# Kernel tuning notes

Measured on AMD Instinct MI355X. Metric: run time of the kernel, lower is better.

The kernel has to match this reference:

```python
import jax, jax.numpy as jnp
import numpy as np

N = 16_777_216  # number of draft tokens / cache slots
ACCEPT_PROB = 0.7


def setup_inputs() -> dict:
    key = jax.random.key(0)
    k1, k2, k3 = jax.random.split(key, 3)
    idx = jax.random.randint(k1, (N,), 0, N, dtype=jnp.int64)
    keep = jax.random.uniform(k2, (N,)) < ACCEPT_PROB
    # rejected slots are marked -1, as in the original kernel
    accept_index = jnp.where(keep, idx, jnp.int64(-1))
    out_cache_loc = jax.random.normal(k3, (N,), dtype=jnp.float32)
    return {"accept_index": accept_index, "out_cache_loc": out_cache_loc}


def reference(accept_index, out_cache_loc):
    """Stream compaction: gather out_cache_loc[accept_index[i]] for every i with
    accept_index[i] >= 0, packed densely at the front of the output.

    The original returns an array of length num_accepted (data-dependent). For a
    static, jit-compatible shape we return a length-N array whose first
    num_accepted entries equal the original output and the rest are zero.
    """
    n = accept_index.shape[0]
    mask = accept_index >= 0                      # [N] bool
    # exclusive prefix sum of mask = destination slot for each accepted element
    dst = jnp.cumsum(mask.astype(jnp.int64)) - mask.astype(jnp.int64)  # [N]
    # gather (use 0 as a safe dummy index for rejected lanes)
    vals = out_cache_loc[jnp.where(mask, accept_index, 0)]             # [N]
    # scatter accepted values to their compacted slots; rejected lanes are
    # routed to index n, which mode='drop' discards
    scatter_idx = jnp.where(mask, dst, n)
    out = jnp.zeros((n,), dtype=out_cache_loc.dtype)
    out = out.at[scatter_idx].set(vals, mode="drop")
    return out
```

## Files before the change

### kernel.cpp

```cpp
#include <hip/hip_runtime.h>


#define N_TOTAL  16777216
#define BLOCK    256
#define EPT2     32
#define TILE2    (BLOCK * EPT2)
#define NB2      (N_TOTAL / TILE2)
#define SLICE_LG 20
#define SLICES   16

#define EPT      16
#define TILE     (BLOCK * EPT)
#define NBLOCKS  (N_TOTAL / TILE)
#define SLICE_LG5 22
#define SLICES5  (N_TOTAL >> SLICE_LG5)

typedef float vfloat4 __attribute__((ext_vector_type(4)));

__global__ __launch_bounds__(BLOCK) void k_count(const int* __restrict__ idx,
                                                 int* __restrict__ cnt) {
    __shared__ int h[SLICES];
    const int b = blockIdx.x, t = threadIdx.x;
    if (t < SLICES) h[t] = 0;
    __syncthreads();
    const int4* p = (const int4*)(idx + (size_t)b * TILE2 + (size_t)t * EPT2);
    int v[EPT2];
#pragma unroll
    for (int j = 0; j < EPT2 / 4; ++j) {
        int4 q = p[j];
        v[4*j+0]=q.x; v[4*j+1]=q.y; v[4*j+2]=q.z; v[4*j+3]=q.w;
    }
#pragma unroll
    for (int j = 0; j < EPT2; ++j) {
        unsigned s = (unsigned)v[j] >> SLICE_LG;
        if (s < SLICES) atomicAdd(&h[s], 1);
    }
    __syncthreads();
    if (t < SLICES) cnt[b * SLICES + t] = h[t];
}

__global__ __launch_bounds__(BLOCK) void k_scan2(const int* __restrict__ cnt,
                                                 int* __restrict__ off,
                                                 int* __restrict__ sliceBase,
                                                 int* __restrict__ blockOff) {
    const int t = threadIdx.x, lane = t & 63, wave = t >> 6;
    const int R = NB2 / BLOCK;
    int sum[SLICES];
#pragma unroll
    for (int s = 0; s < SLICES; ++s) sum[s] = 0;
    for (int r = 0; r < R; ++r) {
        const int4* row = (const int4*)(cnt + (size_t)(t * R + r) * SLICES);
        int4 c0 = row[0], c1 = row[1], c2 = row[2], c3 = row[3];
        sum[0]+=c0.x; sum[1]+=c0.y; sum[2]+=c0.z; sum[3]+=c0.w;
        sum[4]+=c1.x; sum[5]+=c1.y; sum[6]+=c1.z; sum[7]+=c1.w;
        sum[8]+=c2.x; sum[9]+=c2.y; sum[10]+=c2.z; sum[11]+=c2.w;
        sum[12]+=c3.x; sum[13]+=c3.y; sum[14]+=c3.z; sum[15]+=c3.w;
    }
    int inc[SLICES];
#pragma unroll
    for (int s = 0; s < SLICES; ++s) inc[s] = sum[s];
#pragma unroll
    for (int d = 1; d < 64; d <<= 1) {
#pragma unroll
        for (int s = 0; s < SLICES; ++s) {
            int u = __shfl_up(inc[s], d);
            if (lane >= d) inc[s] += u;
        }
    }
    int tTot = 0;
#pragma unroll
    for (int s = 0; s < SLICES; ++s) tTot += sum[s];
    int tInc = tTot;
#pragma unroll
    for (int d = 1; d < 64; d <<= 1) {
        int u = __shfl_up(tInc, d);
        if (lane >= d) tInc += u;
    }
    __shared__ int wtot[4][SLICES], wstot[4];
    __shared__ int wbase[4][SLICES], wsbase[4];
    if (lane == 63) {
#pragma unroll
        for (int s = 0; s < SLICES; ++s) wtot[wave][s] = inc[s];
        wstot[wave] = tInc;
    }
    __syncthreads();
    if (t == 0) {
        int run[SLICES];
#pragma unroll
        for (int s = 0; s < SLICES; ++s) run[s] = 0;
        for (int w = 0; w < 4; ++w)
#pragma unroll
            for (int s = 0; s < SLICES; ++s) { wbase[w][s] = run[s]; run[s] += wtot[w][s]; }
        int sr = 0;
#pragma unroll
        for (int s = 0; s < SLICES; ++s) { sliceBase[s] = sr; sr += run[s]; }
        sliceBase[SLICES] = sr;
        blockOff[NB2] = sr;
        int rs = 0;
        for (int w = 0; w < 4; ++w) { wsbase[w] = rs; rs += wstot[w]; }
    }
    __syncthreads();
    int ex[SLICES];
#pragma unroll
    for (int s = 0; s < SLICES; ++s) ex[s] = inc[s] - sum[s] + wbase[wave][s];
    int exA = tInc - tTot + wsbase[wave];
    for (int r = 0; r < R; ++r) {
        const int b = t * R + r;
        blockOff[b] = exA;
        const int4* row = (const int4*)(cnt + (size_t)b * SLICES);
        int4 c0 = row[0], c1 = row[1], c2 = row[2], c3 = row[3];
        int rv[SLICES] = {c0.x,c0.y,c0.z,c0.w, c1.x,c1.y,c1.z,c1.w,
                          c2.x,c2.y,c2.z,c2.w, c3.x,c3.y,c3.z,c3.w};
#pragma unroll
        for (int s = 0; s < SLICES; ++s) {
            off[(size_t)b * SLICES + s] = ex[s];
            ex[s] += rv[s];
            exA   += rv[s];
        }
    }
}

__global__ __launch_bounds__(BLOCK) void k_bin(const int* __restrict__ idx,
                                               const int* __restrict__ off,
                                               const int* __restrict__ sliceBase,
                                               int* __restrict__ bins) {
    const int b = blockIdx.x, t = threadIdx.x, lane = t & 63, wave = t >> 6;
    const int4* p = (const int4*)(idx + (size_t)b * TILE2 + (size_t)t * EPT2);
    int v[EPT2];
#pragma unroll
    for (int j = 0; j < EPT2 / 4; ++j) {
        int4 q = p[j];
        v[4*j+0]=q.x; v[4*j+1]=q.y; v[4*j+2]=q.z; v[4*j+3]=q.w;
    }
    int tc[SLICES];
#pragma unroll
    for (int s = 0; s < SLICES; ++s) tc[s] = 0;
#pragma unroll
    for (int j = 0; j < EPT2; ++j) {
        unsigned s = (unsigned)v[j] >> SLICE_LG;
#pragma unroll
        for (int s2 = 0; s2 < SLICES; ++s2) tc[s2] += (s == (unsigned)s2);
    }
    int inc[SLICES];
#pragma unroll
    for (int s = 0; s < SLICES; ++s) inc[s] = tc[s];
#pragma unroll
    for (int d = 1; d < 64; d <<= 1) {
#pragma unroll
        for (int s = 0; s < SLICES; ++s) {
            int u = __shfl_up(inc[s], d);
            if (lane >= d) inc[s] += u;
        }
    }
    __shared__ int wtot[4][SLICES], wbase[4][SLICES];
    __shared__ int gbase[SLICES], segStart[SLICES + 1];
    if (lane == 63)
#pragma unroll
        for (int s = 0; s < SLICES; ++s) wtot[wave][s] = inc[s];
    __syncthreads();
    if (t == 0) {
        int run[SLICES];
#pragma unroll
        for (int s = 0; s < SLICES; ++s) run[s] = 0;
        for (int w = 0; w < 4; ++w)
#pragma unroll
            for (int s = 0; s < SLICES; ++s) { wbase[w][s] = run[s]; run[s] += wtot[w][s]; }
        int sr = 0;
#pragma unroll
        for (int s = 0; s < SLICES; ++s) { segStart[s] = sr; sr += run[s]; }
        segStart[SLICES] = sr;
#pragma unroll
        for (int s = 0; s < SLICES; ++s)
            gbase[s] = sliceBase[s] + off[(size_t)b * SLICES + s] - segStart[s];
    }
    __syncthreads();
    __shared__ int exb[BLOCK][SLICES + 1];
    __shared__ int binsBuf[TILE2];
#pragma unroll
    for (int s = 0; s < SLICES; ++s)
        exb[t][s] = segStart[s] + (inc[s] - tc[s]) + wbase[wave][s];
#pragma unroll
    for (int j = 0; j < EPT2; ++j) {
        unsigned s = (unsigned)v[j] >> SLICE_LG;
        if (s < SLICES) {
            int pLoc = exb[t][s]++;
            binsBuf[pLoc] = v[j];
        }
    }
    __syncthreads();
    const int tot = segStart[SLICES];
    for (int k = t; k < tot; k += BLOCK) {
        int x = binsBuf[k];
        int s = 0;
#pragma unroll
        for (int q = 1; q < SLICES; ++q) s += (k >= segStart[q]);
        __builtin_nontemporal_store(x, bins + gbase[s] + k);
    }
}

__global__ __launch_bounds__(BLOCK) void k_gather(const int* __restrict__ bins,
                                                  const float* __restrict__ src,
                                                  const int* __restrict__ sliceBase,
                                                  float* __restrict__ val) {
    __shared__ int pad[18432];
    const int t = threadIdx.x;
    pad[t] = t;
    const int n = blockIdx.x;
    const int x = n & 7;
    const int g = n >> 9;
    const int q = (n >> 3) & 63;
    const int s = 2 * x + (g >> 1);
    const int c = (g & 1) * 64 + q;
    const int s0 = sliceBase[s], s1 = sliceBase[s + 1];
    if (s1 == -1) val[0] = (float)pad[t];
    const int len = s1 - s0;
    const int L = (len + 127) >> 7;
    const int start = s0 + c * L;
    const int end = (start + L < s1) ? (start + L) : s1;
    for (int k0 = start + t; k0 < end; k0 += BLOCK * 8) {
        int kk[8], bm[8];
        float fm[8];
#pragma unroll
        for (int m = 0; m < 8; ++m) kk[m] = k0 + m * BLOCK;
#pragma unroll
        for (int m = 0; m < 8; ++m) {
            int kc = kk[m] < end ? kk[m] : end - 1;
            bm[m] = __builtin_nontemporal_load(bins + kc);
        }
#pragma unroll
        for (int m = 0; m < 8; ++m) fm[m] = src[bm[m]];
#pragma unroll
        for (int m = 0; m < 8; ++m)
            if (kk[m] < end) __builtin_nontemporal_store(fm[m], val + kk[m]);
    }
}

__global__ __launch_bounds__(BLOCK) void k_emit(const int* __restrict__ idx,
                                                const int* __restrict__ off,
                                                const int* __restrict__ sliceBase,
                                                const int* __restrict__ blockOff,
                                                const float* __restrict__ val,
                                                float* __restrict__ out) {
    const int b = blockIdx.x, t = threadIdx.x, lane = t & 63, wave = t >> 6;
    const int4* p = (const int4*)(idx + (size_t)b * TILE2 + (size_t)t * EPT2);
    int v[EPT2];
#pragma unroll
    for (int j = 0; j < EPT2 / 4; ++j) {
        int4 q = p[j];
        v[4*j+0]=q.x; v[4*j+1]=q.y; v[4*j+2]=q.z; v[4*j+3]=q.w;
    }
    int tc[SLICES];
#pragma unroll
    for (int s = 0; s < SLICES; ++s) tc[s] = 0;
#pragma unroll
    for (int j = 0; j < EPT2; ++j) {
        unsigned s = (unsigned)v[j] >> SLICE_LG;
#pragma unroll
        for (int s2 = 0; s2 < SLICES; ++s2) tc[s2] += (s == (unsigned)s2);
    }
    int inc[SLICES];
#pragma unroll
    for (int s = 0; s < SLICES; ++s) inc[s] = tc[s];
#pragma unroll
    for (int d = 1; d < 64; d <<= 1) {
#pragma unroll
        for (int s = 0; s < SLICES; ++s) {
            int u = __shfl_up(inc[s], d);
            if (lane >= d) inc[s] += u;
        }
    }
    int cnt = 0;
#pragma unroll
    for (int s = 0; s < SLICES; ++s) cnt += tc[s];
    int xinc = cnt;
#pragma unroll
    for (int d = 1; d < 64; d <<= 1) {
        int u = __shfl_up(xinc, d);
        if (lane >= d) xinc += u;
    }
    __shared__ int wtot[4][SLICES], wbase[4][SLICES];
    __shared__ int wsum[4], woff[4], sTot;
    if (lane == 63) {
#pragma unroll
        for (int s = 0; s < SLICES; ++s) wtot[wave][s] = inc[s];
        wsum[wave] = xinc;
    }
    __syncthreads();
    if (t == 0) {
        int run[SLICES];
#pragma unroll
        for (int s = 0; s < SLICES; ++s) run[s] = 0;
        for (int w = 0; w < 4; ++w)
#pragma unroll
            for (int s = 0; s < SLICES; ++s) { wbase[w][s] = run[s]; run[s] += wtot[w][s]; }
        int rs = 0;
        for (int w = 0; w < 4; ++w) { woff[w] = rs; rs += wsum[w]; }
        sTot = rs;
    }
    __syncthreads();
    __shared__ int exb[BLOCK][SLICES + 1];
#pragma unroll
    for (int s = 0; s < SLICES; ++s)
        exb[t][s] = sliceBase[s] + off[(size_t)b * SLICES + s]
                  + (inc[s] - tc[s]) + wbase[wave][s];
    int slotA[EPT2];
#pragma unroll
    for (int j = 0; j < EPT2; ++j) {
        unsigned s = (unsigned)v[j] >> SLICE_LG;
        slotA[j] = (s < SLICES) ? exb[t][s]++ : 0;
    }
    float tmp[EPT2];
#pragma unroll
    for (int j = 0; j < EPT2; ++j) tmp[j] = val[slotA[j]];
    __shared__ float vals[TILE2];
    int o = (xinc - cnt) + woff[wave];
#pragma unroll
    for (int j = 0; j < EPT2; ++j)
        if (v[j] >= 0) vals[o++] = tmp[j];
    __syncthreads();
    const int base = blockOff[b];
    const int tot = sTot;
    for (int i = t; i < tot; i += BLOCK)
        __builtin_nontemporal_store(vals[i], out + base + i);
}

__global__ __launch_bounds__(256) void k_tail(float* __restrict__ out,
                                              const int* __restrict__ total_p) {
    const int total = *total_p;
    const int i = (blockIdx.x * 256 + threadIdx.x) * 4;
    if (i >= total) {
        vfloat4 z = (vfloat4)(0.f);
        __builtin_nontemporal_store(z, (vfloat4*)(out + i));
    } else if (i + 4 > total) {
#pragma unroll
        for (int k = 0; k < 4; ++k)
            if (i + k >= total) out[i + k] = 0.f;
    }
}

__global__ __launch_bounds__(BLOCK) void k_reduce(const int* __restrict__ idx,
                                                  int* __restrict__ blockSums) {
    const int b = blockIdx.x, t = threadIdx.x;
    const int4* p = (const int4*)(idx + (size_t)b * TILE + (size_t)t * EPT);
    int cnt = 0;
#pragma unroll
    for (int j = 0; j < EPT / 4; ++j) {
        int4 v = p[j];
        cnt += (v.x >= 0) + (v.y >= 0) + (v.z >= 0) + (v.w >= 0);
    }
#pragma unroll
    for (int d = 32; d > 0; d >>= 1) cnt += __shfl_down(cnt, d);
    __shared__ int wsum[BLOCK / 64];
    const int lane = t & 63, wave = t >> 6;
    if (lane == 0) wsum[wave] = cnt;
    __syncthreads();
    if (t == 0) {
        int s = 0;
#pragma unroll
        for (int w = 0; w < BLOCK / 64; ++w) s += wsum[w];
        blockSums[b] = s;
    }
}

__global__ __launch_bounds__(256) void k_scan(const int* __restrict__ blockSums,
                                              int* __restrict__ blockOffsets) {
    const int t = threadIdx.x;
    const int lane = t & 63, wave = t >> 6;
    int vals[16];
    const int4* p = (const int4*)(blockSums + t * 16);
#pragma unroll
    for (int j = 0; j < 4; ++j) {
        int4 v = p[j];
        vals[4*j+0]=v.x; vals[4*j+1]=v.y; vals[4*j+2]=v.z; vals[4*j+3]=v.w;
    }
    int tsum = 0;
#pragma unroll
    for (int j = 0; j < 16; ++j) tsum += vals[j];
    int x = tsum;
#pragma unroll
    for (int d = 1; d < 64; d <<= 1) {
        int y = __shfl_up(x, d);
        if (lane >= d) x += y;
    }
    __shared__ int wsum[4], woff[4];
    if (lane == 63) wsum[wave] = x;
    __syncthreads();
    if (t == 0) {
        int s = 0;
#pragma unroll
        for (int w = 0; w < 4; ++w) { woff[w] = s; s += wsum[w]; }
        blockOffsets[NBLOCKS] = s;
    }
    __syncthreads();
    int run = (x - tsum) + woff[wave];
#pragma unroll
    for (int j = 0; j < 16; ++j) {
        blockOffsets[t * 16 + j] = run;
        run += vals[j];
    }
}

__global__ __launch_bounds__(BLOCK) void k_scatter(const int* __restrict__ idx,
                                                   const float* __restrict__ src,
                                                   const int* __restrict__ blockOffsets,
                                                   float* __restrict__ out) {
    const int b = blockIdx.x, t = threadIdx.x;
    const int lane = t & 63, wave = t >> 6;
    const int4* p = (const int4*)(idx + (size_t)b * TILE2 + (size_t)t * EPT2);
    int v[EPT2];
#pragma unroll
    for (int j = 0; j < EPT2 / 4; ++j) {
        int4 q = p[j];
        v[4*j+0]=q.x; v[4*j+1]=q.y; v[4*j+2]=q.z; v[4*j+3]=q.w;
    }
    int cnt = 0;
#pragma unroll
    for (int j = 0; j < EPT2; ++j) cnt += (v[j] >= 0);
    int x = cnt;
#pragma unroll
    for (int d = 1; d < 64; d <<= 1) {
        int y = __shfl_up(x, d);
        if (lane >= d) x += y;
    }
    __shared__ int wsum[BLOCK / 64], woff[BLOCK / 64];
    __shared__ int btotal;
    if (lane == 63) wsum[wave] = x;
    __syncthreads();
    if (t == 0) {
        int s = 0;
#pragma unroll
        for (int w = 0; w < BLOCK / 64; ++w) { woff[w] = s; s += wsum[w]; }
        btotal = s;
    }
    __syncthreads();
    const int off0 = (x - cnt) + woff[wave];
    __shared__ float vals[TILE2];
#pragma unroll 1
    for (int s = 0; s < SLICES5; ++s) {
        float tmp[EPT2];
#pragma unroll
        for (int j = 0; j < EPT2; ++j) {
            const bool m = (int)((unsigned)v[j] >> SLICE_LG5) == s;
            tmp[j] = src[m ? v[j] : 0];
        }
        asm volatile("s_waitcnt vmcnt(0)" ::: "memory");
        int o = off0;
#pragma unroll
        for (int j = 0; j < EPT2; ++j) {
            const bool acc = v[j] >= 0;
            const bool m = (int)((unsigned)v[j] >> SLICE_LG5) == s;
            if (m) vals[o] = tmp[j];
            o += acc;
        }
    }
    __syncthreads();
    const int base = blockOffsets[2 * b];
    const int tot  = btotal;
    for (int i = t; i < tot; i += BLOCK)
        __builtin_nontemporal_store(vals[i], out + base + i);
}

extern "C" void kernel_launch(void* const* d_in, const int* in_sizes, int n_in,
                              void* d_out, int out_size, void* d_ws, size_t ws_size,
                              hipStream_t stream) {
    const int*   idx = (const int*)d_in[0];
    const float* src = (const float*)d_in[1];
    float*       out = (float*)d_out;

    int* cnt       = (int*)d_ws;
    int* off       = cnt + NB2 * SLICES;
    int* sliceBase = off + NB2 * SLICES;
    int* blockOff  = sliceBase + (SLICES + 1);
    int* bins      = blockOff + (NB2 + 1);
    float* val     = (float*)(bins + N_TOTAL);
    const size_t need = ((size_t)(2 * NB2 * SLICES + SLICES + 1 + NB2 + 1)
                         + 2ull * N_TOTAL) * 4ull;

    if (ws_size >= need) {
        k_count <<<NB2, BLOCK, 0, stream>>>(idx, cnt);
        k_scan2 <<<1, BLOCK, 0, stream>>>(cnt, off, sliceBase, blockOff);
        k_bin   <<<NB2, BLOCK, 0, stream>>>(idx, off, sliceBase, bins);
        k_gather<<<NB2, BLOCK, 0, stream>>>(bins, src, sliceBase, val);
        k_emit  <<<NB2, BLOCK, 0, stream>>>(idx, off, sliceBase, blockOff, val, out);
        k_tail  <<<N_TOTAL / 4 / 256, 256, 0, stream>>>(out, blockOff + NB2);
    } else {
        int* blockSums    = (int*)d_ws;
        int* blockOffsets = blockSums + NBLOCKS;
        k_reduce <<<NBLOCKS, BLOCK, 0, stream>>>(idx, blockSums);
        k_scan   <<<1, 256, 0, stream>>>(blockSums, blockOffsets);
        k_scatter<<<NB2, BLOCK, 0, stream>>>(idx, src, blockOffsets, out);
        k_tail   <<<N_TOTAL / 4 / 256, 256, 0, stream>>>(out, blockOffsets + NBLOCKS);
    }
}
```

Baseline: 369.2 us.

## Replace LDS atomics histogram with register counts and shrink gather grid

k_count now builds per-thread slice counts in registers and reduces them with wave shuffles plus a small shared array, replacing shared-memory atomicAdd contention. k_gather drops the 72KB shared padding array that had been limiting occupancy, and launches 512 blocks that each loop over four slice/chunk groups instead of 2048 blocks with one group each. This trades fewer resident blocks per launch for higher occupancy per CU and removes the padding trick. The register histogram adds compare-add work proportional to SLICES times elements per thread.

```diff
diff --git a/kernel.cpp b/kernel.cpp
--- a/kernel.cpp
+++ b/kernel.cpp
@@ -8,6 +8,7 @@
 #define NB2      (N_TOTAL / TILE2)
 #define SLICE_LG 20
 #define SLICES   16
+#define GBLOCKS  512
 
 #define EPT      16
 #define TILE     (BLOCK * EPT)
@@ -19,10 +20,7 @@
 
 __global__ __launch_bounds__(BLOCK) void k_count(const int* __restrict__ idx,
                                                  int* __restrict__ cnt) {
-    __shared__ int h[SLICES];
-    const int b = blockIdx.x, t = threadIdx.x;
-    if (t < SLICES) h[t] = 0;
-    __syncthreads();
+    const int b = blockIdx.x, t = threadIdx.x, lane = t & 63, wave = t >> 6;
     const int4* p = (const int4*)(idx + (size_t)b * TILE2 + (size_t)t * EPT2);
     int v[EPT2];
 #pragma unroll
@@ -30,13 +28,26 @@
         int4 q = p[j];
         v[4*j+0]=q.x; v[4*j+1]=q.y; v[4*j+2]=q.z; v[4*j+3]=q.w;
     }
+    int tc[SLICES];
+#pragma unroll
+    for (int s = 0; s < SLICES; ++s) tc[s] = 0;
 #pragma unroll
     for (int j = 0; j < EPT2; ++j) {
         unsigned s = (unsigned)v[j] >> SLICE_LG;
-        if (s < SLICES) atomicAdd(&h[s], 1);
-    }
-    __syncthreads();
-    if (t < SLICES) cnt[b * SLICES + t] = h[t];
+#pragma unroll
+        for (int s2 = 0; s2 < SLICES; ++s2) tc[s2] += (s == (unsigned)s2);
+    }
+#pragma unroll
+    for (int s = 0; s < SLICES; ++s)
+#pragma unroll
+        for (int d = 32; d > 0; d >>= 1) tc[s] += __shfl_down(tc[s], d);
+    __shared__ int ws[4][SLICES];
+    if (lane == 0)
+#pragma unroll
+        for (int s = 0; s < SLICES; ++s) ws[wave][s] = tc[s];
+    __syncthreads();
+    if (t < SLICES)
+        cnt[b * SLICES + t] = ws[0][t] + ws[1][t] + ws[2][t] + ws[3][t];
 }
 
 __global__ __launch_bounds__(BLOCK) void k_scan2(const int* __restrict__ cnt,
@@ -202,36 +213,35 @@
                                                   const float* __restrict__ src,
                                                   const int* __restrict__ sliceBase,
                                                   float* __restrict__ val) {
-    __shared__ int pad[18432];
     const int t = threadIdx.x;
-    pad[t] = t;
     const int n = blockIdx.x;
     const int x = n & 7;
-    const int g = n >> 9;
     const int q = (n >> 3) & 63;
-    const int s = 2 * x + (g >> 1);
-    const int c = (g & 1) * 64 + q;
-    const int s0 = sliceBase[s], s1 = sliceBase[s + 1];
-    if (s1 == -1) val[0] = (float)pad[t];
-    const int len = s1 - s0;
-    const int L = (len + 127) >> 7;
-    const int start = s0 + c * L;
-    const int end = (start + L < s1) ? (start + L) : s1;
-    for (int k0 = start + t; k0 < end; k0 += BLOCK * 8) {
-        int kk[8], bm[8];
-        float fm[8];
-#pragma unroll
-        for (int m = 0; m < 8; ++m) kk[m] = k0 + m * BLOCK;
-#pragma unroll
-        for (int m = 0; m < 8; ++m) {
-            int kc = kk[m] < end ? kk[m] : end - 1;
-            bm[m] = __builtin_nontemporal_load(bins + kc);
-        }
-#pragma unroll
-        for (int m = 0; m < 8; ++m) fm[m] = src[bm[m]];
-#pragma unroll
-        for (int m = 0; m < 8; ++m)
-            if (kk[m] < end) __builtin_nontemporal_store(fm[m], val + kk[m]);
+#pragma unroll 1
+    for (int g = 0; g < 4; ++g) {
+        const int s = 2 * x + (g >> 1);
+        const int c = (g & 1) * 64 + q;
+        const int s0 = sliceBase[s], s1 = sliceBase[s + 1];
+        const int len = s1 - s0;
+        const int L = (len + 127) >> 7;
+        const int start = s0 + c * L;
+        const int end = (start + L < s1) ? (start + L) : s1;
+        for (int k0 = start + t; k0 < end; k0 += BLOCK * 8) {
+            int kk[8], bm[8];
+            float fm[8];
+#pragma unroll
+            for (int m = 0; m < 8; ++m) kk[m] = k0 + m * BLOCK;
+#pragma unroll
+            for (int m = 0; m < 8; ++m) {
+                int kc = kk[m] < end ? kk[m] : end - 1;
+                bm[m] = __builtin_nontemporal_load(bins + kc);
+            }
+#pragma unroll
+            for (int m = 0; m < 8; ++m) fm[m] = src[bm[m]];
+#pragma unroll
+            for (int m = 0; m < 8; ++m)
+                if (kk[m] < end) __builtin_nontemporal_store(fm[m], val + kk[m]);
+        }
     }
 }
 
@@ -480,7 +490,7 @@
         k_count <<<NB2, BLOCK, 0, stream>>>(idx, cnt);
         k_scan2 <<<1, BLOCK, 0, stream>>>(cnt, off, sliceBase, blockOff);
         k_bin   <<<NB2, BLOCK, 0, stream>>>(idx, off, sliceBase, bins);
-        k_gather<<<NB2, BLOCK, 0, stream>>>(bins, src, sliceBase, val);
+        k_gather<<<GBLOCKS, BLOCK, 0, stream>>>(bins, src, sliceBase, val);
         k_emit  <<<NB2, BLOCK, 0, stream>>>(idx, off, sliceBase, blockOff, val, out);
         k_tail  <<<N_TOTAL / 4 / 256, 256, 0, stream>>>(out, blockOff + NB2);
     } else {
```

Measured after the change: 367.7 us. No clear change (-0.4%).
